# Kernel optimization log

Measured on AMD Instinct MI355X. Metric: run time of the kernel, lower is better.

The kernel has to match this reference:

```python
import jax, jax.numpy as jnp
import numpy as np

B, S, D = 16, 2048, 512
E, TOP_K = 8, 2
H = 4 * D  # expert hidden dim


def setup_inputs() -> dict:
    key = jax.random.key(0)
    ks = jax.random.split(key, 8)
    x = jax.random.normal(ks[0], (B, S, D), dtype=jnp.float32)
    gate_w = jax.random.normal(ks[1], (D, E), dtype=jnp.float32) * 0.02
    gate_b = jnp.zeros((E,), dtype=jnp.float32)
    w1 = jax.random.normal(ks[2], (E, D, H), dtype=jnp.float32) * 0.02
    b1 = jnp.zeros((E, H), dtype=jnp.float32)
    w2 = jax.random.normal(ks[3], (E, H, D), dtype=jnp.float32) * 0.02
    b2 = jnp.zeros((E, D), dtype=jnp.float32)
    return {"x": x, "gate_w": gate_w, "gate_b": gate_b,
            "w1": w1, "b1": b1, "w2": w2, "b2": b2}


def reference(x, gate_w, gate_b, w1, b1, w2, b2):
    # Sample-level top-k routing (mean pooling over sequence).
    b, s, d = x.shape
    e = gate_b.shape[0]
    pooled = x.mean(axis=1)                       # [B, D]
    logits = pooled @ gate_w + gate_b             # [B, E]
    top_v, top_i = jax.lax.top_k(logits, TOP_K)   # [B, K]
    weights = jax.nn.softmax(top_v, axis=-1)      # [B, K]
    # Dense per-sample-per-expert combine weight; zero for unselected experts,
    # which makes the dense expert evaluation below mathematically identical
    # to the masked gather/scatter in the torch module.
    w_full = jnp.zeros((b, e), dtype=x.dtype).at[jnp.arange(b)[:, None], top_i].add(weights)
    out = jnp.zeros_like(x)
    for ex in range(e):  # small fixed expert loop
        h = jax.nn.gelu(x @ w1[ex] + b1[ex], approximate=False)  # torch GELU default = exact erf
        y = h @ w2[ex] + b2[ex]  # Dropout(0.1) is identity in eval mode
        out = out + y * w_full[:, ex][:, None, None]
    return out
```

## Files before the change

kernel.cpp:

```cpp
#include <hip/hip_runtime.h>
#include <hip/hip_bf16.h>
#include <math.h>

#define B_ 16
#define S_ 2048
#define D_ 512
#define E_ 8
#define H_ 2048

typedef __bf16 bf16_t;
typedef __bf16 bf16x8 __attribute__((ext_vector_type(8)));
typedef __bf16 bf16x4v __attribute__((ext_vector_type(4)));
typedef float f32x4 __attribute__((ext_vector_type(4)));

__device__ __forceinline__ void gload_lds16(const void* g, void* l) {
  __builtin_amdgcn_global_load_lds((const __attribute__((address_space(1))) void*)g,
                                   (__attribute__((address_space(3))) void*)l,
                                   16, 0, 0);
}

#define BAR() __builtin_amdgcn_s_barrier()
#define LGKM0() do { asm volatile("s_waitcnt lgkmcnt(0)" ::: "memory"); \
                     __builtin_amdgcn_sched_barrier(0); } while (0)
#define LGKMW() asm volatile("s_waitcnt lgkmcnt(0)" ::: "memory")
#define LGKM8() asm volatile("s_waitcnt lgkmcnt(8)" ::: "memory")
#define VM4() asm volatile("s_waitcnt vmcnt(4)" ::: "memory")
#define VM0() asm volatile("s_waitcnt vmcnt(0)" ::: "memory")
#define PRIO1() __builtin_amdgcn_s_setprio(1)
#define PRIO0() __builtin_amdgcn_s_setprio(0)

__device__ __forceinline__ float fast_gelu(float v) {
  const float t = 1.5957691216f * v * (1.0f + 0.044715f * v * v);
  return v * __builtin_amdgcn_rcpf(1.0f + __expf(-t));
}

__global__ void prep_kernel(const float* __restrict__ x, bf16_t* __restrict__ xbf,
                            float* __restrict__ pool,
                            const float* __restrict__ w1, bf16_t* __restrict__ w1t,
                            const float* __restrict__ w2, bf16_t* __restrict__ w2t) {
  const int id = blockIdx.x;
  const int tid = threadIdx.x;
  if (id < 256) {
    const int ch = id & 15, b = id >> 4;
    const int cg = tid & 127;
    const int rg = tid >> 7;
    const size_t base = ((size_t)b * S_ + (size_t)ch * 128 + rg * 32) * D_ + cg * 4;
    const float* xp = x + base;
    bf16_t* op = xbf + base;
    float s0 = 0.f, s1 = 0.f, s2 = 0.f, s3 = 0.f;
#pragma unroll 4
    for (int r = 0; r < 32; ++r) {
      float4 v = *reinterpret_cast<const float4*>(xp + (size_t)r * D_);
      s0 += v.x; s1 += v.y; s2 += v.z; s3 += v.w;
      bf16x4v o;
      o[0] = (bf16_t)v.x; o[1] = (bf16_t)v.y; o[2] = (bf16_t)v.z; o[3] = (bf16_t)v.w;
      *reinterpret_cast<bf16x4v*>(op + (size_t)r * D_) = o;
    }
    float* pp = pool + ((size_t)b * 64 + ch * 4 + rg) * D_ + cg * 4;
    pp[0] = s0; pp[1] = s1; pp[2] = s2; pp[3] = s3;
    return;
  }
  int t = id - 256;
  const float* in; bf16_t* outp; int R, C, r0, c0;
  if (t < 1024) {
    const int e = t >> 7, u = t & 127;
    R = D_; C = H_;
    r0 = (u >> 4) * 64; c0 = (u & 15) * 128;
    in = w1 + (size_t)e * R * C; outp = w1t + (size_t)e * R * C;
  } else {
    t -= 1024;
    const int e = t >> 7, u = t & 127;
    R = H_; C = D_;
    r0 = (u >> 2) * 64; c0 = (u & 3) * 128;
    in = w2 + (size_t)e * R * C; outp = w2t + (size_t)e * R * C;
  }
  const int cb2 = tid >> 4;
  const int rb  = tid & 15;
  const float* ip = in + (size_t)(r0 + rb * 4) * C + c0 + cb2 * 4;
  f32x4 v0 = *reinterpret_cast<const f32x4*>(ip);
  f32x4 v1 = *reinterpret_cast<const f32x4*>(ip + C);
  f32x4 v2 = *reinterpret_cast<const f32x4*>(ip + 2 * C);
  f32x4 v3 = *reinterpret_cast<const f32x4*>(ip + 3 * C);
  bf16_t* opb = outp + (size_t)(c0 + cb2 * 4) * R + r0 + rb * 4;
#pragma unroll
  for (int i = 0; i < 4; ++i) {
    bf16x4v o;
    o[0] = (bf16_t)v0[i]; o[1] = (bf16_t)v1[i]; o[2] = (bf16_t)v2[i]; o[3] = (bf16_t)v3[i];
    *reinterpret_cast<bf16x4v*>(opb + (size_t)i * R) = o;
  }
}

__global__ void gate_kernel(const float* __restrict__ pool, const float* __restrict__ gw,
                            const float* __restrict__ gb, int* __restrict__ route_e,
                            float* __restrict__ route_w) {
  const int b = blockIdx.x;
  const int d = threadIdx.x;
  const int lane = d & 63, wave = d >> 6;
  float p = 0.f;
#pragma unroll
  for (int c = 0; c < 64; ++c) p += pool[((size_t)b * 64 + c) * D_ + d];
  p *= (1.0f / (float)S_);

  __shared__ float wsum[8][8];
  __shared__ float logits[E_];
#pragma unroll
  for (int e = 0; e < E_; ++e) {
    float v = p * gw[d * E_ + e];
#pragma unroll
    for (int off = 32; off >= 1; off >>= 1) v += __shfl_xor(v, off);
    if (lane == 0) wsum[wave][e] = v;
  }
  __syncthreads();
  if (d < E_) {
    float l = gb[d];
#pragma unroll
    for (int w = 0; w < 8; ++w) l += wsum[w][d];
    logits[d] = l;
  }
  __syncthreads();
  if (d == 0) {
    int i0 = 0; float v0 = logits[0];
    for (int e = 1; e < E_; ++e) if (logits[e] > v0) { v0 = logits[e]; i0 = e; }
    int i1 = -1; float v1 = -3.0e38f;
    for (int e = 0; e < E_; ++e) if (e != i0 && logits[e] > v1) { v1 = logits[e]; i1 = e; }
    const float z = expf(v1 - v0);
    const float inv = 1.0f / (1.0f + z);
    route_e[2 * b] = i0; route_e[2 * b + 1] = i1;
    route_w[2 * b] = inv; route_w[2 * b + 1] = z * inv;
  }
}

#define GEMM_THREAD_CONSTS() \
  const int tid = threadIdx.x; \
  const int lane = tid & 63; \
  const int wave = tid >> 6; \
  const int wr = wave >> 2; \
  const int wc = wave & 3; \
  const int fl = lane & 15; \
  const int hi = (lane >> 4) & 3; \
  const int flb = fl * 128; \
  const int xorv = (fl & 7) << 4; \
  const int koff0 = (hi * 16) ^ xorv; \
  const int koff1 = (64 + hi * 16) ^ xorv; \
  const int r0s = tid >> 3; \
  const int g0s = ((tid & 7) ^ (r0s & 7)) << 3; \
  const int r1s = 64 + (tid >> 3); \
  const int g1s = ((tid & 7) ^ (r1s & 7)) << 3;

#define STAGE_HALF(g, ld, row0, col0, lo) do { \
  gload_lds16((g) + (size_t)((row0) + r0s) * (ld) + (col0) + g0s, smem + (lo) + tid * 16); \
  gload_lds16((g) + (size_t)((row0) + r1s) * (ld) + (col0) + g1s, smem + (lo) + 8192 + tid * 16); \
} while (0)

#define RD_A(mh) do { \
  const char* _pA = smem + ((((t) & 1) * 2 + wr) << 14); \
  _Pragma("unroll") for (int mq = 0; mq < 4; ++mq) { \
    a[mq][0] = *reinterpret_cast<const bf16x8*>(_pA + (mh) * 8192 + mq * 2048 + flb + koff0); \
    a[mq][1] = *reinterpret_cast<const bf16x8*>(_pA + (mh) * 8192 + mq * 2048 + flb + koff1); \
  } } while (0)

#define RD_B(nh) do { \
  const char* _pB = smem + 65536 + ((((t) & 1) * 2 + (wc >> 1)) << 14) + ((wc & 1) << 13); \
  _Pragma("unroll") for (int nq = 0; nq < 2; ++nq) { \
    bb[nh][nq][0] = *reinterpret_cast<const bf16x8*>(_pB + (nh) * 4096 + nq * 2048 + flb + koff0); \
    bb[nh][nq][1] = *reinterpret_cast<const bf16x8*>(_pB + (nh) * 4096 + nq * 2048 + flb + koff1); \
  } } while (0)

#define MFMA_Q(mh, nh) do { \
  _Pragma("unroll") for (int mq = 0; mq < 4; ++mq) \
  _Pragma("unroll") for (int nq = 0; nq < 2; ++nq) { \
    acc[(mh)*4+mq][(nh)*2+nq] = __builtin_amdgcn_mfma_f32_16x16x32_bf16( \
        a[mq][0], bb[nh][nq][0], acc[(mh)*4+mq][(nh)*2+nq], 0, 0, 0); \
    acc[(mh)*4+mq][(nh)*2+nq] = __builtin_amdgcn_mfma_f32_16x16x32_bf16( \
        a[mq][1], bb[nh][nq][1], acc[(mh)*4+mq][(nh)*2+nq], 0, 0, 0); \
  } } while (0)

__global__ __launch_bounds__(512, 2) void gemm1_kernel(
    const bf16_t* __restrict__ xbf, const bf16_t* __restrict__ w1t,
    const float* __restrict__ b1, const int* __restrict__ route_e,
    bf16_t* __restrict__ h_ws, int g0) {
  __shared__ alignas(16) char smem[131072];
  const int nwg = gridDim.x;
  const int id = blockIdx.x;
  const int swz = (id & 7) * (nwg >> 3) + (id >> 3);
  const int lg = swz >> 6;
  const int tile = swz & 63;
  const int m0 = (tile >> 3) * 256;
  const int n0 = (tile & 7) * 256;
  const int g = g0 + lg;
  const int b = g >> 1;
  const int e = route_e[g];
  const bf16_t* Ax = xbf + (size_t)b * S_ * D_;
  const bf16_t* Bw = w1t + (size_t)e * H_ * D_;
  bf16_t* C = h_ws + (size_t)lg * S_ * H_;

  GEMM_THREAD_CONSTS();

  f32x4 acc[8][4];
#pragma unroll
  for (int i = 0; i < 8; ++i)
#pragma unroll
    for (int j = 0; j < 4; ++j) acc[i][j] = f32x4{0.f, 0.f, 0.f, 0.f};
  bf16x8 a[4][2], bb[2][2][2];

#define ST_A1(tt, hh) STAGE_HALF(Ax, D_, m0 + (hh) * 128, (tt) * 64, ((((tt) & 1) * 2 + (hh)) << 14))
#define ST_B1(tt, hh) STAGE_HALF(Bw, D_, n0 + (hh) * 128, (tt) * 64, 65536 + ((((tt) & 1) * 2 + (hh)) << 14))

  const int NT = D_ / 64;
  ST_A1(0, 0); ST_A1(0, 1); ST_B1(0, 0); ST_B1(0, 1);
  ST_B1(1, 0); ST_B1(1, 1);
  VM4(); BAR();

  for (int t = 0; t < NT; ++t) {
    RD_A(0); RD_B(0);
    if (t + 1 < NT) ST_A1(t + 1, 0);
    BAR(); LGKM0(); PRIO1(); MFMA_Q(0, 0); PRIO0(); BAR();
    RD_B(1);
    if (t + 1 < NT) ST_A1(t + 1, 1);
    BAR(); LGKM0(); PRIO1(); MFMA_Q(0, 1); PRIO0(); BAR();
    RD_A(1);
    if (t + 2 < NT) ST_B1(t + 2, 0);
    BAR(); LGKM0(); PRIO1(); MFMA_Q(1, 0); PRIO0(); BAR();
    if (t + 2 < NT) ST_B1(t + 2, 1);
    if (t < NT - 2) { VM4(); } else if (t == NT - 2) { VM0(); }
    BAR(); PRIO1(); MFMA_Q(1, 1); PRIO0(); BAR();
  }
#undef ST_A1
#undef ST_B1

  const int rb2 = hi * 4;
#pragma unroll
  for (int ni = 0; ni < 4; ++ni) {
    const int col = wc * 64 + ni * 16 + fl;
    const float bias = b1[e * H_ + n0 + col];
    const int cb = col * 2;
#pragma unroll
    for (int mi = 0; mi < 8; ++mi) {
#pragma unroll
      for (int j = 0; j < 4; ++j) {
        const int row = wr * 128 + mi * 16 + rb2 + j;
        const float v = acc[mi][ni][j] + bias;
        const int ad = (row << 9) + (cb ^ (((row >> 2) & 3) << 5));
        *reinterpret_cast<bf16_t*>(smem + ad) = (bf16_t)fast_gelu(v);
      }
    }
  }
  LGKMW(); BAR();
#pragma unroll
  for (int i = 0; i < 16; ++i) {
    const int byte = i * 8192 + tid * 16;
    const int row = byte >> 9;
    const int colb = byte & 511;
    const int ad = (row << 9) + (colb ^ (((row >> 2) & 3) << 5));
    const bf16x8 vv = *reinterpret_cast<const bf16x8*>(smem + ad);
    *reinterpret_cast<bf16x8*>((char*)C + ((size_t)(m0 + row) * H_ + n0) * 2 + colb) = vv;
  }
}

__global__ __launch_bounds__(512, 2) void gemm2_kernel(
    const bf16_t* __restrict__ h_ws, const bf16_t* __restrict__ w2t,
    const float* __restrict__ b2, const int* __restrict__ route_e,
    const float* __restrict__ route_w, float* __restrict__ out, int b0) {
  __shared__ alignas(16) char smem[131072];
  const int nwg = gridDim.x;
  const int id = blockIdx.x;
  const int swz = (id & 7) * (nwg >> 3) + (id >> 3);
  const int lb = swz >> 4;
  const int tile = swz & 15;
  const int m0 = (tile >> 1) * 256;
  const int n0 = (tile & 1) * 256;
  const int smp = b0 + lb;
  const int e0 = route_e[2 * smp], e1 = route_e[2 * smp + 1];
  const float wg0 = route_w[2 * smp], wg1 = route_w[2 * smp + 1];
  const float ratio = wg1 / wg0;
  const bf16_t* Ae1 = h_ws + (size_t)(lb * 2 + 1) * S_ * H_;
  const bf16_t* Ae0 = h_ws + (size_t)(lb * 2 + 0) * S_ * H_;
  const bf16_t* Be1 = w2t + (size_t)e1 * D_ * H_;
  const bf16_t* Be0 = w2t + (size_t)e0 * D_ * H_;

  GEMM_THREAD_CONSTS();

  f32x4 acc[8][4];
#pragma unroll
  for (int i = 0; i < 8; ++i)
#pragma unroll
    for (int j = 0; j < 4; ++j) acc[i][j] = f32x4{0.f, 0.f, 0.f, 0.f};
  bf16x8 a[4][2], bb[2][2][2];

#define ST_A2(tt, hh) do { const bf16_t* _ab = ((tt) < 32) ? Ae1 : Ae0; \
  STAGE_HALF(_ab, H_, m0 + (hh) * 128, ((tt) & 31) * 64, ((((tt) & 1) * 2 + (hh)) << 14)); } while (0)
#define ST_B2(tt, hh) do { const bf16_t* _bbp = ((tt) < 32) ? Be1 : Be0; \
  STAGE_HALF(_bbp, H_, n0 + (hh) * 128, ((tt) & 31) * 64, 65536 + ((((tt) & 1) * 2 + (hh)) << 14)); } while (0)

  const int NT = 64;
  ST_A2(0, 0); ST_A2(0, 1); ST_B2(0, 0); ST_B2(0, 1);
  ST_B2(1, 0); ST_B2(1, 1);
  VM4(); BAR();

  for (int t = 0; t < NT; ++t) {
    RD_A(0); RD_B(0);
    if (t + 1 < NT) ST_A2(t + 1, 0);
    LGKM8(); BAR(); LGKM0(); PRIO1(); MFMA_Q(0, 0); PRIO0(); BAR();
    RD_B(1);
    if (t + 1 < NT) ST_A2(t + 1, 1);
    BAR(); LGKM0(); PRIO1(); MFMA_Q(0, 1); PRIO0(); BAR();
    RD_A(1);
    if (t + 2 < NT) ST_B2(t + 2, 0);
    BAR(); LGKM0(); PRIO1(); MFMA_Q(1, 0); PRIO0(); BAR();
    if (t + 2 < NT) ST_B2(t + 2, 1);
    if (t < NT - 2) { VM4(); } else if (t == NT - 2) { VM0(); }
    BAR(); PRIO1(); MFMA_Q(1, 1); PRIO0();
    if (t == 31) {
#pragma unroll
      for (int i = 0; i < 8; ++i)
#pragma unroll
        for (int j = 0; j < 4; ++j) acc[i][j] = acc[i][j] * ratio;
    }
    BAR();
  }
#undef ST_A2
#undef ST_B2

  const int rb2 = hi * 4;
  float* Co = out + (size_t)smp * S_ * D_;
#pragma unroll
  for (int ni = 0; ni < 4; ++ni) {
    const int gc = n0 + wc * 64 + ni * 16 + fl;
    const float wb = wg0 * b2[e0 * D_ + gc] + wg1 * b2[e1 * D_ + gc];
#pragma unroll
    for (int mi = 0; mi < 8; ++mi) {
#pragma unroll
      for (int j = 0; j < 4; ++j) {
        const int gr = m0 + wr * 128 + mi * 16 + rb2 + j;
        Co[(size_t)gr * D_ + gc] = wg0 * acc[mi][ni][j] + wb;
      }
    }
  }
}

extern "C" void kernel_launch(void* const* d_in, const int* in_sizes, int n_in,
                              void* d_out, int out_size, void* d_ws, size_t ws_size,
                              hipStream_t stream) {
  const float* x      = (const float*)d_in[0];
  const float* gate_w = (const float*)d_in[1];
  const float* gate_b = (const float*)d_in[2];
  const float* w1     = (const float*)d_in[3];
  const float* b1     = (const float*)d_in[4];
  const float* w2     = (const float*)d_in[5];
  const float* b2     = (const float*)d_in[6];
  float* out = (float*)d_out;
  char* ws = (char*)d_ws;

  bf16_t* xbf    = (bf16_t*)(ws);
  bf16_t* w1t    = (bf16_t*)(ws + 33554432);
  bf16_t* w2t    = (bf16_t*)(ws + 50331648);
  float*  pool   = (float*)(ws + 67108864);
  int*    route_e = (int*)(ws + 69206016);
  float*  route_w = (float*)(ws + 69206144);
  const size_t h_off = 69206272;
  bf16_t* h_ws   = (bf16_t*)(ws + h_off);

  const size_t per_b = (size_t)2 * S_ * H_ * sizeof(bf16_t);
  size_t avail = (ws_size > h_off) ? (ws_size - h_off) : 0;
  int nb = (int)(avail / per_b);
  if (nb < 1) nb = 1;
  if (nb > B_) nb = B_;

  prep_kernel<<<2304, 512, 0, stream>>>(x, xbf, pool, w1, w1t, w2, w2t);
  gate_kernel<<<B_, 512, 0, stream>>>(pool, gate_w, gate_b, route_e, route_w);

  for (int b0 = 0; b0 < B_; b0 += nb) {
    const int cb = (B_ - b0 < nb) ? (B_ - b0) : nb;
    gemm1_kernel<<<64 * cb * 2, 512, 0, stream>>>(xbf, w1t, b1, route_e, h_ws, b0 * 2);
    gemm2_kernel<<<16 * cb, 512, 0, stream>>>(h_ws, w2t, b2, route_e, route_w, out, b0);
  }
}
```

Measured before the change: 465.3 us.

## Split hidden dimension in halves so every sample runs in one GEMM pass

Measured after the change: 398.8 us. 14.3% less time.

```diff
diff --git a/kernel.cpp b/kernel.cpp
--- a/kernel.cpp
+++ b/kernel.cpp
@@ -175,24 +175,26 @@
         a[mq][1], bb[nh][nq][1], acc[(mh)*4+mq][(nh)*2+nq], 0, 0, 0); \
   } } while (0)
 
+template<int NTN>
 __global__ __launch_bounds__(512, 2) void gemm1_kernel(
     const bf16_t* __restrict__ xbf, const bf16_t* __restrict__ w1t,
     const float* __restrict__ b1, const int* __restrict__ route_e,
-    bf16_t* __restrict__ h_ws, int g0) {
+    bf16_t* __restrict__ h_ws, int g0, int nbase, int ldc) {
   __shared__ alignas(16) char smem[131072];
+  const int TILES = 8 * NTN;
   const int nwg = gridDim.x;
   const int id = blockIdx.x;
   const int swz = (id & 7) * (nwg >> 3) + (id >> 3);
-  const int lg = swz >> 6;
-  const int tile = swz & 63;
-  const int m0 = (tile >> 3) * 256;
-  const int n0 = (tile & 7) * 256;
+  const int lg = swz / TILES;
+  const int tile = swz % TILES;
+  const int m0 = (tile / NTN) * 256;
+  const int n0 = (tile % NTN) * 256;
   const int g = g0 + lg;
   const int b = g >> 1;
   const int e = route_e[g];
   const bf16_t* Ax = xbf + (size_t)b * S_ * D_;
   const bf16_t* Bw = w1t + (size_t)e * H_ * D_;
-  bf16_t* C = h_ws + (size_t)lg * S_ * H_;
+  bf16_t* C = h_ws + (size_t)lg * S_ * ldc;
 
   GEMM_THREAD_CONSTS();
 
@@ -204,7 +206,7 @@
   bf16x8 a[4][2], bb[2][2][2];
 
 #define ST_A1(tt, hh) STAGE_HALF(Ax, D_, m0 + (hh) * 128, (tt) * 64, ((((tt) & 1) * 2 + (hh)) << 14))
-#define ST_B1(tt, hh) STAGE_HALF(Bw, D_, n0 + (hh) * 128, (tt) * 64, 65536 + ((((tt) & 1) * 2 + (hh)) << 14))
+#define ST_B1(tt, hh) STAGE_HALF(Bw, D_, nbase + n0 + (hh) * 128, (tt) * 64, 65536 + ((((tt) & 1) * 2 + (hh)) << 14))
 
   const int NT = D_ / 64;
   ST_A1(0, 0); ST_A1(0, 1); ST_B1(0, 0); ST_B1(0, 1);
@@ -232,7 +234,7 @@
 #pragma unroll
   for (int ni = 0; ni < 4; ++ni) {
     const int col = wc * 64 + ni * 16 + fl;
-    const float bias = b1[e * H_ + n0 + col];
+    const float bias = b1[e * H_ + nbase + n0 + col];
     const int cb = col * 2;
 #pragma unroll
     for (int mi = 0; mi < 8; ++mi) {
@@ -253,14 +255,16 @@
     const int colb = byte & 511;
     const int ad = (row << 9) + (colb ^ (((row >> 2) & 3) << 5));
     const bf16x8 vv = *reinterpret_cast<const bf16x8*>(smem + ad);
-    *reinterpret_cast<bf16x8*>((char*)C + ((size_t)(m0 + row) * H_ + n0) * 2 + colb) = vv;
-  }
-}
-
+    *reinterpret_cast<bf16x8*>((char*)C + ((size_t)(m0 + row) * ldc + n0) * 2 + colb) = vv;
+  }
+}
+
+template<int KNT, bool ADD>
 __global__ __launch_bounds__(512, 2) void gemm2_kernel(
     const bf16_t* __restrict__ h_ws, const bf16_t* __restrict__ w2t,
     const float* __restrict__ b2, const int* __restrict__ route_e,
-    const float* __restrict__ route_w, float* __restrict__ out, int b0) {
+    const float* __restrict__ route_w, float* __restrict__ out, int b0,
+    int lda, int kbase) {
   __shared__ alignas(16) char smem[131072];
   const int nwg = gridDim.x;
   const int id = blockIdx.x;
@@ -273,8 +277,8 @@
   const int e0 = route_e[2 * smp], e1 = route_e[2 * smp + 1];
   const float wg0 = route_w[2 * smp], wg1 = route_w[2 * smp + 1];
   const float ratio = wg1 / wg0;
-  const bf16_t* Ae1 = h_ws + (size_t)(lb * 2 + 1) * S_ * H_;
-  const bf16_t* Ae0 = h_ws + (size_t)(lb * 2 + 0) * S_ * H_;
+  const bf16_t* Ae1 = h_ws + (size_t)(lb * 2 + 1) * S_ * lda;
+  const bf16_t* Ae0 = h_ws + (size_t)(lb * 2 + 0) * S_ * lda;
   const bf16_t* Be1 = w2t + (size_t)e1 * D_ * H_;
   const bf16_t* Be0 = w2t + (size_t)e0 * D_ * H_;
 
@@ -287,12 +291,14 @@
     for (int j = 0; j < 4; ++j) acc[i][j] = f32x4{0.f, 0.f, 0.f, 0.f};
   bf16x8 a[4][2], bb[2][2][2];
 
-#define ST_A2(tt, hh) do { const bf16_t* _ab = ((tt) < 32) ? Ae1 : Ae0; \
-  STAGE_HALF(_ab, H_, m0 + (hh) * 128, ((tt) & 31) * 64, ((((tt) & 1) * 2 + (hh)) << 14)); } while (0)
-#define ST_B2(tt, hh) do { const bf16_t* _bbp = ((tt) < 32) ? Be1 : Be0; \
-  STAGE_HALF(_bbp, H_, n0 + (hh) * 128, ((tt) & 31) * 64, 65536 + ((((tt) & 1) * 2 + (hh)) << 14)); } while (0)
-
-  const int NT = 64;
+  const int KH = KNT / 2;
+
+#define ST_A2(tt, hh) do { const bf16_t* _ab = ((tt) < KH) ? Ae1 : Ae0; \
+  STAGE_HALF(_ab, lda, m0 + (hh) * 128, ((tt) & (KH - 1)) * 64, ((((tt) & 1) * 2 + (hh)) << 14)); } while (0)
+#define ST_B2(tt, hh) do { const bf16_t* _bbp = ((tt) < KH) ? Be1 : Be0; \
+  STAGE_HALF(_bbp, H_, n0 + (hh) * 128, kbase + ((tt) & (KH - 1)) * 64, 65536 + ((((tt) & 1) * 2 + (hh)) << 14)); } while (0)
+
+  const int NT = KNT;
   ST_A2(0, 0); ST_A2(0, 1); ST_B2(0, 0); ST_B2(0, 1);
   ST_B2(1, 0); ST_B2(1, 1);
   VM4(); BAR();
@@ -310,7 +316,7 @@
     if (t + 2 < NT) ST_B2(t + 2, 1);
     if (t < NT - 2) { VM4(); } else if (t == NT - 2) { VM0(); }
     BAR(); PRIO1(); MFMA_Q(1, 1); PRIO0();
-    if (t == 31) {
+    if (t == KH - 1) {
 #pragma unroll
       for (int i = 0; i < 8; ++i)
 #pragma unroll
@@ -326,13 +332,15 @@
 #pragma unroll
   for (int ni = 0; ni < 4; ++ni) {
     const int gc = n0 + wc * 64 + ni * 16 + fl;
-    const float wb = wg0 * b2[e0 * D_ + gc] + wg1 * b2[e1 * D_ + gc];
+    const float wb = ADD ? 0.f : (wg0 * b2[e0 * D_ + gc] + wg1 * b2[e1 * D_ + gc]);
 #pragma unroll
     for (int mi = 0; mi < 8; ++mi) {
 #pragma unroll
       for (int j = 0; j < 4; ++j) {
         const int gr = m0 + wr * 128 + mi * 16 + rb2 + j;
-        Co[(size_t)gr * D_ + gc] = wg0 * acc[mi][ni][j] + wb;
+        const size_t idx = (size_t)gr * D_ + gc;
+        const float base = ADD ? Co[idx] : wb;
+        Co[idx] = base + wg0 * acc[mi][ni][j];
       }
     }
   }
@@ -360,18 +368,25 @@
   const size_t h_off = 69206272;
   bf16_t* h_ws   = (bf16_t*)(ws + h_off);
 
-  const size_t per_b = (size_t)2 * S_ * H_ * sizeof(bf16_t);
-  size_t avail = (ws_size > h_off) ? (ws_size - h_off) : 0;
-  int nb = (int)(avail / per_b);
-  if (nb < 1) nb = 1;
-  if (nb > B_) nb = B_;
-
   prep_kernel<<<2304, 512, 0, stream>>>(x, xbf, pool, w1, w1t, w2, w2t);
   gate_kernel<<<B_, 512, 0, stream>>>(pool, gate_w, gate_b, route_e, route_w);
 
-  for (int b0 = 0; b0 < B_; b0 += nb) {
-    const int cb = (B_ - b0 < nb) ? (B_ - b0) : nb;
-    gemm1_kernel<<<64 * cb * 2, 512, 0, stream>>>(xbf, w1t, b1, route_e, h_ws, b0 * 2);
-    gemm2_kernel<<<16 * cb, 512, 0, stream>>>(h_ws, w2t, b2, route_e, route_w, out, b0);
-  }
-}
+  const bool split = ws_size >= h_off + (size_t)134217728;
+  if (split) {
+    gemm1_kernel<4><<<1024, 512, 0, stream>>>(xbf, w1t, b1, route_e, h_ws, 0, 0, 1024);
+    gemm2_kernel<32, false><<<256, 512, 0, stream>>>(h_ws, w2t, b2, route_e, route_w, out, 0, 1024, 0);
+    gemm1_kernel<4><<<1024, 512, 0, stream>>>(xbf, w1t, b1, route_e, h_ws, 0, 1024, 1024);
+    gemm2_kernel<32, true><<<256, 512, 0, stream>>>(h_ws, w2t, b2, route_e, route_w, out, 0, 1024, 1024);
+  } else {
+    const size_t per_b = (size_t)2 * S_ * H_ * sizeof(bf16_t);
+    size_t avail = (ws_size > h_off) ? (ws_size - h_off) : 0;
+    int nb = (int)(avail / per_b);
+    if (nb < 1) nb = 1;
+    if (nb > B_) nb = B_;
+    for (int b0 = 0; b0 < B_; b0 += nb) {
+      const int cb = (B_ - b0 < nb) ? (B_ - b0) : nb;
+      gemm1_kernel<8><<<64 * cb * 2, 512, 0, stream>>>(xbf, w1t, b1, route_e, h_ws, b0 * 2, 0, H_);
+      gemm2_kernel<64, false><<<16 * cb, 512, 0, stream>>>(h_ws, w2t, b2, route_e, route_w, out, b0, H_, 0);
+    }
+  }
+}
```

## Split sequence into halves with smaller gemm2 tiles to raise occupancy

Applied to the files above, without the earlier changes.

After: 391.9 us. 1.19x faster.

```diff
diff --git a/kernel.cpp b/kernel.cpp
--- a/kernel.cpp
+++ b/kernel.cpp
@@ -175,24 +175,26 @@
         a[mq][1], bb[nh][nq][1], acc[(mh)*4+mq][(nh)*2+nq], 0, 0, 0); \
   } } while (0)
 
+template<int NTM, int NTN>
 __global__ __launch_bounds__(512, 2) void gemm1_kernel(
     const bf16_t* __restrict__ xbf, const bf16_t* __restrict__ w1t,
     const float* __restrict__ b1, const int* __restrict__ route_e,
-    bf16_t* __restrict__ h_ws, int g0) {
+    bf16_t* __restrict__ h_ws, int g0, int mbase, size_t cstride) {
   __shared__ alignas(16) char smem[131072];
+  const int TILES = NTM * NTN;
   const int nwg = gridDim.x;
   const int id = blockIdx.x;
   const int swz = (id & 7) * (nwg >> 3) + (id >> 3);
-  const int lg = swz >> 6;
-  const int tile = swz & 63;
-  const int m0 = (tile >> 3) * 256;
-  const int n0 = (tile & 7) * 256;
+  const int lg = swz / TILES;
+  const int tile = swz % TILES;
+  const int m0 = (tile / NTN) * 256;
+  const int n0 = (tile % NTN) * 256;
   const int g = g0 + lg;
   const int b = g >> 1;
   const int e = route_e[g];
   const bf16_t* Ax = xbf + (size_t)b * S_ * D_;
   const bf16_t* Bw = w1t + (size_t)e * H_ * D_;
-  bf16_t* C = h_ws + (size_t)lg * S_ * H_;
+  bf16_t* C = h_ws + (size_t)lg * cstride;
 
   GEMM_THREAD_CONSTS();
 
@@ -203,7 +205,7 @@
     for (int j = 0; j < 4; ++j) acc[i][j] = f32x4{0.f, 0.f, 0.f, 0.f};
   bf16x8 a[4][2], bb[2][2][2];
 
-#define ST_A1(tt, hh) STAGE_HALF(Ax, D_, m0 + (hh) * 128, (tt) * 64, ((((tt) & 1) * 2 + (hh)) << 14))
+#define ST_A1(tt, hh) STAGE_HALF(Ax, D_, mbase + m0 + (hh) * 128, (tt) * 64, ((((tt) & 1) * 2 + (hh)) << 14))
 #define ST_B1(tt, hh) STAGE_HALF(Bw, D_, n0 + (hh) * 128, (tt) * 64, 65536 + ((((tt) & 1) * 2 + (hh)) << 14))
 
   const int NT = D_ / 64;
@@ -214,7 +216,7 @@
   for (int t = 0; t < NT; ++t) {
     RD_A(0); RD_B(0);
     if (t + 1 < NT) ST_A1(t + 1, 0);
-    BAR(); LGKM0(); PRIO1(); MFMA_Q(0, 0); PRIO0(); BAR();
+    LGKM8(); BAR(); LGKM0(); PRIO1(); MFMA_Q(0, 0); PRIO0(); BAR();
     RD_B(1);
     if (t + 1 < NT) ST_A1(t + 1, 1);
     BAR(); LGKM0(); PRIO1(); MFMA_Q(0, 1); PRIO0(); BAR();
@@ -257,6 +259,112 @@
   }
 }
 
+template<int KNT>
+__global__ __launch_bounds__(512, 2) void gemm2s_kernel(
+    const bf16_t* __restrict__ h_ws, const bf16_t* __restrict__ w2t,
+    const float* __restrict__ b2, const int* __restrict__ route_e,
+    const float* __restrict__ route_w, float* __restrict__ out, int srow) {
+  __shared__ alignas(16) char smem[98304];
+  const int nwg = gridDim.x;
+  const int id = blockIdx.x;
+  const int swz = (id & 7) * (nwg >> 3) + (id >> 3);
+  const int lb = swz >> 4;
+  const int tile = swz & 15;
+  const int m0 = (tile >> 1) * 128;
+  const int n0 = (tile & 1) * 256;
+  const int e0 = route_e[2 * lb], e1 = route_e[2 * lb + 1];
+  const float wg0 = route_w[2 * lb], wg1 = route_w[2 * lb + 1];
+  const float ratio = wg1 / wg0;
+  const bf16_t* Ae1 = h_ws + (size_t)(lb * 2 + 1) * 1024 * H_;
+  const bf16_t* Ae0 = h_ws + (size_t)(lb * 2 + 0) * 1024 * H_;
+  const bf16_t* Be1 = w2t + (size_t)e1 * D_ * H_;
+  const bf16_t* Be0 = w2t + (size_t)e0 * D_ * H_;
+
+  GEMM_THREAD_CONSTS();
+  (void)koff1;
+
+  f32x4 acc[4][4];
+#pragma unroll
+  for (int i = 0; i < 4; ++i)
+#pragma unroll
+    for (int j = 0; j < 4; ++j) acc[i][j] = f32x4{0.f, 0.f, 0.f, 0.f};
+  bf16x8 a[4][2], bb[2][2][2];
+
+  const int KH = KNT / 2;
+
+#define ST_A2S(tt) do { const bf16_t* _ab = ((tt) < KH) ? Ae1 : Ae0; \
+  STAGE_HALF(_ab, H_, m0, ((tt) & (KH - 1)) * 64, (((tt) & 1) << 14)); } while (0)
+#define ST_B2S(tt, hh) do { const bf16_t* _bbp = ((tt) < KH) ? Be1 : Be0; \
+  STAGE_HALF(_bbp, H_, n0 + (hh) * 128, ((tt) & (KH - 1)) * 64, 32768 + ((((tt) & 1) * 2 + (hh)) << 14)); } while (0)
+
+#define RD_AS() do { \
+  const char* _pA = smem + (((t) & 1) << 14); \
+  _Pragma("unroll") for (int mq = 0; mq < 4; ++mq) { \
+    a[mq][0] = *reinterpret_cast<const bf16x8*>(_pA + wr * 8192 + mq * 2048 + flb + koff0); \
+    a[mq][1] = *reinterpret_cast<const bf16x8*>(_pA + wr * 8192 + mq * 2048 + flb + koff1); \
+  } } while (0)
+
+#define RD_BS(nh) do { \
+  const char* _pB = smem + 32768 + ((((t) & 1) * 2 + (wc >> 1)) << 14) + ((wc & 1) << 13); \
+  _Pragma("unroll") for (int nq = 0; nq < 2; ++nq) { \
+    bb[nh][nq][0] = *reinterpret_cast<const bf16x8*>(_pB + (nh) * 4096 + nq * 2048 + flb + koff0); \
+    bb[nh][nq][1] = *reinterpret_cast<const bf16x8*>(_pB + (nh) * 4096 + nq * 2048 + flb + koff1); \
+  } } while (0)
+
+#define MFMA_S(nh) do { \
+  _Pragma("unroll") for (int mq = 0; mq < 4; ++mq) \
+  _Pragma("unroll") for (int nq = 0; nq < 2; ++nq) { \
+    acc[mq][(nh)*2+nq] = __builtin_amdgcn_mfma_f32_16x16x32_bf16( \
+        a[mq][0], bb[nh][nq][0], acc[mq][(nh)*2+nq], 0, 0, 0); \
+    acc[mq][(nh)*2+nq] = __builtin_amdgcn_mfma_f32_16x16x32_bf16( \
+        a[mq][1], bb[nh][nq][1], acc[mq][(nh)*2+nq], 0, 0, 0); \
+  } } while (0)
+
+  const int NT = KNT;
+  ST_A2S(0); ST_B2S(0, 0); ST_B2S(0, 1);
+  ST_B2S(1, 0); ST_B2S(1, 1);
+  VM4(); BAR();
+
+  for (int t = 0; t < NT; ++t) {
+    RD_AS(); RD_BS(0);
+    if (t + 1 < NT) ST_A2S(t + 1);
+    LGKM8(); BAR(); LGKM0(); PRIO1(); MFMA_S(0); PRIO0(); BAR();
+    RD_BS(1);
+    if (t + 2 < NT) { ST_B2S(t + 2, 0); ST_B2S(t + 2, 1); }
+    if (t < NT - 2) { VM4(); } else if (t == NT - 2) { VM0(); }
+    BAR(); LGKM0(); PRIO1(); MFMA_S(1); PRIO0();
+    if (t == KH - 1) {
+#pragma unroll
+      for (int i = 0; i < 4; ++i)
+#pragma unroll
+        for (int j = 0; j < 4; ++j) acc[i][j] = acc[i][j] * ratio;
+    }
+    BAR();
+  }
+#undef ST_A2S
+#undef ST_B2S
+#undef RD_AS
+#undef RD_BS
+#undef MFMA_S
+
+  const int rb2 = hi * 4;
+  float* Co = out + (size_t)lb * S_ * D_;
+#pragma unroll
+  for (int ni = 0; ni < 4; ++ni) {
+    const int gc = n0 + wc * 64 + ni * 16 + fl;
+    const float wb = wg0 * b2[e0 * D_ + gc] + wg1 * b2[e1 * D_ + gc];
+#pragma unroll
+    for (int mq = 0; mq < 4; ++mq) {
+#pragma unroll
+      for (int j = 0; j < 4; ++j) {
+        const int gr = srow + m0 + wr * 64 + mq * 16 + rb2 + j;
+        Co[(size_t)gr * D_ + gc] = wg0 * acc[mq][ni][j] + wb;
+      }
+    }
+  }
+}
+
+template<int KNT>
 __global__ __launch_bounds__(512, 2) void gemm2_kernel(
     const bf16_t* __restrict__ h_ws, const bf16_t* __restrict__ w2t,
     const float* __restrict__ b2, const int* __restrict__ route_e,
@@ -287,12 +395,14 @@
     for (int j = 0; j < 4; ++j) acc[i][j] = f32x4{0.f, 0.f, 0.f, 0.f};
   bf16x8 a[4][2], bb[2][2][2];
 
-#define ST_A2(tt, hh) do { const bf16_t* _ab = ((tt) < 32) ? Ae1 : Ae0; \
-  STAGE_HALF(_ab, H_, m0 + (hh) * 128, ((tt) & 31) * 64, ((((tt) & 1) * 2 + (hh)) << 14)); } while (0)
-#define ST_B2(tt, hh) do { const bf16_t* _bbp = ((tt) < 32) ? Be1 : Be0; \
-  STAGE_HALF(_bbp, H_, n0 + (hh) * 128, ((tt) & 31) * 64, 65536 + ((((tt) & 1) * 2 + (hh)) << 14)); } while (0)
-
-  const int NT = 64;
+  const int KH = KNT / 2;
+
+#define ST_A2(tt, hh) do { const bf16_t* _ab = ((tt) < KH) ? Ae1 : Ae0; \
+  STAGE_HALF(_ab, H_, m0 + (hh) * 128, ((tt) & (KH - 1)) * 64, ((((tt) & 1) * 2 + (hh)) << 14)); } while (0)
+#define ST_B2(tt, hh) do { const bf16_t* _bbp = ((tt) < KH) ? Be1 : Be0; \
+  STAGE_HALF(_bbp, H_, n0 + (hh) * 128, ((tt) & (KH - 1)) * 64, 65536 + ((((tt) & 1) * 2 + (hh)) << 14)); } while (0)
+
+  const int NT = KNT;
   ST_A2(0, 0); ST_A2(0, 1); ST_B2(0, 0); ST_B2(0, 1);
   ST_B2(1, 0); ST_B2(1, 1);
   VM4(); BAR();
@@ -310,7 +420,7 @@
     if (t + 2 < NT) ST_B2(t + 2, 1);
     if (t < NT - 2) { VM4(); } else if (t == NT - 2) { VM0(); }
     BAR(); PRIO1(); MFMA_Q(1, 1); PRIO0();
-    if (t == 31) {
+    if (t == KH - 1) {
 #pragma unroll
       for (int i = 0; i < 8; ++i)
 #pragma unroll
@@ -360,18 +470,25 @@
   const size_t h_off = 69206272;
   bf16_t* h_ws   = (bf16_t*)(ws + h_off);
 
-  const size_t per_b = (size_t)2 * S_ * H_ * sizeof(bf16_t);
-  size_t avail = (ws_size > h_off) ? (ws_size - h_off) : 0;
-  int nb = (int)(avail / per_b);
-  if (nb < 1) nb = 1;
-  if (nb > B_) nb = B_;
-
   prep_kernel<<<2304, 512, 0, stream>>>(x, xbf, pool, w1, w1t, w2, w2t);
   gate_kernel<<<B_, 512, 0, stream>>>(pool, gate_w, gate_b, route_e, route_w);
 
-  for (int b0 = 0; b0 < B_; b0 += nb) {
-    const int cb = (B_ - b0 < nb) ? (B_ - b0) : nb;
-    gemm1_kernel<<<64 * cb * 2, 512, 0, stream>>>(xbf, w1t, b1, route_e, h_ws, b0 * 2);
-    gemm2_kernel<<<16 * cb, 512, 0, stream>>>(h_ws, w2t, b2, route_e, route_w, out, b0);
-  }
-}
+  const bool split = ws_size >= h_off + (size_t)134217728;
+  if (split) {
+    gemm1_kernel<4, 8><<<1024, 512, 0, stream>>>(xbf, w1t, b1, route_e, h_ws, 0, 0, (size_t)1024 * H_);
+    gemm2s_kernel<64><<<256, 512, 0, stream>>>(h_ws, w2t, b2, route_e, route_w, out, 0);
+    gemm1_kernel<4, 8><<<1024, 512, 0, stream>>>(xbf, w1t, b1, route_e, h_ws, 0, 1024, (size_t)1024 * H_);
+    gemm2s_kernel<64><<<256, 512, 0, stream>>>(h_ws, w2t, b2, route_e, route_w, out, 1024);
+  } else {
+    const size_t per_b = (size_t)2 * S_ * H_ * sizeof(bf16_t);
+    size_t avail = (ws_size > h_off) ? (ws_size - h_off) : 0;
+    int nb = (int)(avail / per_b);
+    if (nb < 1) nb = 1;
+    if (nb > B_) nb = B_;
+    for (int b0 = 0; b0 < B_; b0 += nb) {
+      const int cb = (B_ - b0 < nb) ? (B_ - b0) : nb;
+      gemm1_kernel<8, 8><<<64 * cb * 2, 512, 0, stream>>>(xbf, w1t, b1, route_e, h_ws, b0 * 2, 0, (size_t)S_ * H_);
+      gemm2_kernel<64><<<16 * cb, 512, 0, stream>>>(h_ws, w2t, b2, route_e, route_w, out, b0);
+    }
+  }
+}
```
